# Kernel tuning notes

Measured on AMD Instinct MI355X. Metric: run time of the kernel, lower is better.

Reference implementation:

```python
import jax, jax.numpy as jnp
import numpy as np

N_QUBITS = 3
N_LAYERS = 3
BATCH = 524288
N_FEATURES = 8


def _bcast(a, ndim):
    # reshape trailing singleton dims so a broadcasts against a state slice
    return a.reshape(a.shape + (1,) * (ndim - a.ndim))


def _apply_ry(state, q, theta):
    # state: [B, 2, 2, 2] complex; theta: scalar or [B]
    ax = 1 + q
    s0 = jax.lax.index_in_dim(state, 0, ax, keepdims=False)
    s1 = jax.lax.index_in_dim(state, 1, ax, keepdims=False)
    half = theta * 0.5
    c = _bcast(jnp.cos(half), s0.ndim)
    s = _bcast(jnp.sin(half), s0.ndim)
    n0 = c * s0 - s * s1
    n1 = s * s0 + c * s1
    return jnp.stack([n0, n1], axis=ax)


def _apply_rz(state, q, phi):
    ax = 1 + q
    s0 = jax.lax.index_in_dim(state, 0, ax, keepdims=False)
    s1 = jax.lax.index_in_dim(state, 1, ax, keepdims=False)
    p0 = _bcast(jnp.exp(-0.5j * phi.astype(jnp.complex64)), s0.ndim)
    p1 = _bcast(jnp.exp(0.5j * phi.astype(jnp.complex64)), s1.ndim)
    return jnp.stack([p0 * s0, p1 * s1], axis=ax)


def _apply_cnot(state, c, t):
    ax_c = 1 + c
    s0 = jax.lax.index_in_dim(state, 0, ax_c, keepdims=False)
    s1 = jax.lax.index_in_dim(state, 1, ax_c, keepdims=False)
    ax_t = 1 + t - (1 if t > c else 0)  # target axis after removing control axis
    s1 = jnp.flip(s1, axis=ax_t)  # X on target where control == 1
    return jnp.stack([s0, s1], axis=ax_c)


def _vqc(x, w):
    # x: [B, F] angles, w: [3, 3, 2] weights -> [B, 1] <Z_0>
    B, F = x.shape
    state = jnp.zeros((B, 2, 2, 2), jnp.complex64).at[:, 0, 0, 0].set(1.0)
    # data encoding
    for i in range(N_QUBITS):
        state = _apply_ry(state, i, x[:, i % F])
    # variational layers
    for l in range(N_LAYERS):
        for i in range(N_QUBITS):
            state = _apply_ry(state, i, w[l, i, 0])
            state = _apply_rz(state, i, w[l, i, 1])
        for i in range(N_QUBITS - 1):
            state = _apply_cnot(state, i, i + 1)
    probs = state.real ** 2 + state.imag ** 2  # [B, 2, 2, 2]
    p = probs.sum(axis=(2, 3))  # marginal over qubits 1,2 -> [B, 2]
    out = (p[:, 0] - p[:, 1]).astype(jnp.float32)
    return out[:, None]  # [B, 1]


def setup_inputs() -> dict:
    key = jax.random.key(0)
    kx, kw = jax.random.split(key)
    x = jax.random.normal(kx, (BATCH, N_FEATURES), dtype=jnp.float32)
    q_weights = 0.05 * jax.random.normal(kw, (N_LAYERS, N_QUBITS, 2), dtype=jnp.float32)
    return {"x": x, "q_weights": q_weights}


def reference(x, q_weights):
    return _vqc(x, q_weights)
```

## Files before the change

kernel.cpp:

```cpp
#include <hip/hip_runtime.h>
#include <hip/hip_bf16.h>

__global__ __launch_bounds__(256) void vqc_fused(const float* __restrict__ x,
                                                 const float* __restrict__ w,
                                                 float* __restrict__ out,
                                                 int B) {
    __shared__ float sUr[8][8], sUi[8][8];
    __shared__ float sM[64];

    const int tid = threadIdx.x;

    if (tid < 8) {
        float ar[8], ai[8];
#pragma unroll
        for (int k = 0; k < 8; ++k) {
            ar[k] = (k == tid) ? 1.0f : 0.0f;
            ai[k] = 0.0f;
        }

#pragma unroll
        for (int l = 0; l < 3; ++l) {
#pragma unroll
            for (int i = 0; i < 3; ++i) {
                const int g = l * 3 + i;
                const int m = 1 << (2 - i);

                float s, c;
                __sincosf(0.5f * w[2 * g + 0], &s, &c);
#pragma unroll
                for (int k = 0; k < 8; ++k) {
                    if (k & m) continue;
                    const float a0r = ar[k],     a0i = ai[k];
                    const float a1r = ar[k | m], a1i = ai[k | m];
                    ar[k]     = c * a0r - s * a1r;  ai[k]     = c * a0i - s * a1i;
                    ar[k | m] = s * a0r + c * a1r;  ai[k | m] = s * a0i + c * a1i;
                }

                float sz, cz;
                __sincosf(0.5f * w[2 * g + 1], &sz, &cz);
#pragma unroll
                for (int k = 0; k < 8; ++k) {
                    const float pi = (k & m) ? sz : -sz;
                    const float r  = ar[k] * cz - ai[k] * pi;
                    const float q  = ar[k] * pi + ai[k] * cz;
                    ar[k] = r; ai[k] = q;
                }
            }
#pragma unroll
            for (int k = 4; k <= 5; ++k) {
                const int k2 = k | 2;
                float tr = ar[k]; ar[k] = ar[k2]; ar[k2] = tr;
                float ti = ai[k]; ai[k] = ai[k2]; ai[k2] = ti;
            }
#pragma unroll
            for (int k = 2; k <= 6; k += 4) {
                const int k2 = k | 1;
                float tr = ar[k]; ar[k] = ar[k2]; ar[k2] = tr;
                float ti = ai[k]; ai[k] = ai[k2]; ai[k2] = ti;
            }
        }

#pragma unroll
        for (int k = 0; k < 8; ++k) { sUr[k][tid] = ar[k]; sUi[k][tid] = ai[k]; }
    }
    __syncthreads();

    if (tid < 64) {
        const int a = tid >> 3, b = tid & 7;
        float acc = 0.f;
#pragma unroll
        for (int k = 0; k < 8; ++k) {
            const float z = (k < 4) ? 1.f : -1.f;
            acc += z * (sUr[k][a] * sUr[k][b] + sUi[k][a] * sUi[k][b]);
        }
        sM[tid] = acc;
    }
    __syncthreads();

    const int b = blockIdx.x * blockDim.x + tid;
    if (b >= B) return;

    const float4 xv = *reinterpret_cast<const float4*>(x + (size_t)b * 8);

    float s0, c0, s1, c1, s2, c2;
    __sincosf(0.5f * xv.x, &s0, &c0);
    __sincosf(0.5f * xv.y, &s1, &c1);
    __sincosf(0.5f * xv.z, &s2, &c2);

    const float t0[2] = {c0, s0};
    const float t1[2] = {c1, s1};
    const float t2[2] = {c2, s2};

    float psi[8];
#pragma unroll
    for (int k = 0; k < 8; ++k)
        psi[k] = t0[(k >> 2) & 1] * t1[(k >> 1) & 1] * t2[k & 1];

    float acc = 0.f;
#pragma unroll
    for (int i = 0; i < 8; ++i) {
        float r = 0.f;
#pragma unroll
        for (int j = 0; j < 8; ++j)
            r = fmaf(sM[i * 8 + j], psi[j], r);
        acc = fmaf(psi[i], r, acc);
    }

    out[b] = acc;
}

extern "C" void kernel_launch(void* const* d_in, const int* in_sizes, int n_in,
                              void* d_out, int out_size, void* d_ws, size_t ws_size,
                              hipStream_t stream) {
    const float* x = (const float*)d_in[0];
    const float* w = (const float*)d_in[1];
    float* out = (float*)d_out;

    const int B = out_size;

    vqc_fused<<<(B + 255) / 256, 256, 0, stream>>>(x, w, out, B);
}
```

Before: 11.06 us.

## Process two batch rows per thread and broadcast matrix via readlane

Each thread now evaluates two samples, halving the grid and amortizing the per-block 8x8 unitary precompute over twice as many rows. The 64-entry observable matrix is held one entry per lane and broadcast into scalar registers with readlane instead of repeated LDS loads. Odd B would drop the last sample, and the per-thread loads of x become strided across two rows.

```diff
diff --git a/kernel.cpp b/kernel.cpp
--- a/kernel.cpp
+++ b/kernel.cpp
@@ -4,7 +4,7 @@
 __global__ __launch_bounds__(256) void vqc_fused(const float* __restrict__ x,
                                                  const float* __restrict__ w,
                                                  float* __restrict__ out,
-                                                 int B) {
+                                                 int B2 ) {
     __shared__ float sUr[8][8], sUi[8][8];
     __shared__ float sM[64];
 
@@ -77,36 +77,52 @@
     }
     __syncthreads();
 
-    const int b = blockIdx.x * blockDim.x + tid;
-    if (b >= B) return;
+    const float mv = sM[tid & 63];
 
-    const float4 xv = *reinterpret_cast<const float4*>(x + (size_t)b * 8);
+    const int t = blockIdx.x * blockDim.x + tid;
+    if (t >= B2) return;
 
-    float s0, c0, s1, c1, s2, c2;
-    __sincosf(0.5f * xv.x, &s0, &c0);
-    __sincosf(0.5f * xv.y, &s1, &c1);
-    __sincosf(0.5f * xv.z, &s2, &c2);
+    const float4 xa = *reinterpret_cast<const float4*>(x + (size_t)t * 16);
+    const float4 xb = *reinterpret_cast<const float4*>(x + (size_t)t * 16 + 8);
 
-    const float t0[2] = {c0, s0};
-    const float t1[2] = {c1, s1};
-    const float t2[2] = {c2, s2};
+    float psiA[8], psiB[8];
+    {
+        float s0, c0, s1, c1, s2, c2;
+        __sincosf(0.5f * xa.x, &s0, &c0);
+        __sincosf(0.5f * xa.y, &s1, &c1);
+        __sincosf(0.5f * xa.z, &s2, &c2);
+        const float t0[2] = {c0, s0}, t1[2] = {c1, s1}, t2[2] = {c2, s2};
+#pragma unroll
+        for (int k = 0; k < 8; ++k)
+            psiA[k] = t0[(k >> 2) & 1] * t1[(k >> 1) & 1] * t2[k & 1];
+    }
+    {
+        float s0, c0, s1, c1, s2, c2;
+        __sincosf(0.5f * xb.x, &s0, &c0);
+        __sincosf(0.5f * xb.y, &s1, &c1);
+        __sincosf(0.5f * xb.z, &s2, &c2);
+        const float t0[2] = {c0, s0}, t1[2] = {c1, s1}, t2[2] = {c2, s2};
+#pragma unroll
+        for (int k = 0; k < 8; ++k)
+            psiB[k] = t0[(k >> 2) & 1] * t1[(k >> 1) & 1] * t2[k & 1];
+    }
 
-    float psi[8];
-#pragma unroll
-    for (int k = 0; k < 8; ++k)
-        psi[k] = t0[(k >> 2) & 1] * t1[(k >> 1) & 1] * t2[k & 1];
-
-    float acc = 0.f;
+    float accA = 0.f, accB = 0.f;
 #pragma unroll
     for (int i = 0; i < 8; ++i) {
-        float r = 0.f;
+        float rA = 0.f, rB = 0.f;
 #pragma unroll
-        for (int j = 0; j < 8; ++j)
-            r = fmaf(sM[i * 8 + j], psi[j], r);
-        acc = fmaf(psi[i], r, acc);
+        for (int j = 0; j < 8; ++j) {
+            const float mij = __int_as_float(
+                __builtin_amdgcn_readlane(__float_as_int(mv), i * 8 + j));
+            rA = fmaf(mij, psiA[j], rA);
+            rB = fmaf(mij, psiB[j], rB);
+        }
+        accA = fmaf(psiA[i], rA, accA);
+        accB = fmaf(psiB[i], rB, accB);
     }
 
-    out[b] = acc;
+    *reinterpret_cast<float2*>(out + (size_t)t * 2) = make_float2(accA, accB);
 }
 
 extern "C" void kernel_launch(void* const* d_in, const int* in_sizes, int n_in,
@@ -117,6 +133,7 @@
     float* out = (float*)d_out;
 
     const int B = out_size;
+    const int B2 = B / 2;
 
-    vqc_fused<<<(B + 255) / 256, 256, 0, stream>>>(x, w, out, B);
+    vqc_fused<<<(B2 + 255) / 256, 256, 0, stream>>>(x, w, out, B2);
 }
```

After: 10.35 us. 1.07x faster.
